# Kernel optimization log

Measured on AMD Instinct MI355X. Metric: run time of the kernel, lower is better.

The kernel has to match this reference:

```python
import jax, jax.numpy as jnp
import numpy as np

S, B, N, H = 64, 32, 325, 64

def setup_inputs() -> dict:
    key = jax.random.key(0)
    k1, k2, k3, k4 = jax.random.split(key, 4)
    return {
        "encoder_outputs": jax.random.normal(k1, (S, B, N, H), dtype=jnp.float32),
        "decoder_hidden": jax.random.normal(k2, (B, N, H), dtype=jnp.float32),
        "W": jax.random.normal(k3, (H, H), dtype=jnp.float32) * (1.0 / np.sqrt(H)),
        "b": jax.random.normal(k4, (H,), dtype=jnp.float32) * 0.01,
    }

def reference(encoder_outputs, decoder_hidden, W, b):
    # energy: (S,B,N,H) -- Linear + tanh
    energy = jnp.tanh(jnp.einsum('sbnh,kh->sbnk', encoder_outputs, W) + b)
    # broadcast multiply by decoder_hidden (B,N,H) and reduce over hidden dim -> (S,B,N)
    e = jnp.einsum('sbnh,bnh->sbn', energy, decoder_hidden)
    # softmax over seq_len, output (B,N,S)
    return jax.nn.softmax(jnp.transpose(e, (1, 2, 0)), axis=-1)
```

## Files before the change

### kernel.cpp

```cpp
#include <hip/hip_runtime.h>


constexpr int S = 64, B = 32, N = 325, H = 64;
constexpr int BN = B * N;

typedef __attribute__((ext_vector_type(8))) short short8;
typedef __attribute__((ext_vector_type(4))) float f32x4;

union FragU { unsigned u[4]; short8 s8; };

__device__ inline unsigned pack_hi(float x0, float x1, float& r0, float& r1) {
    unsigned u0 = __builtin_bit_cast(unsigned, x0);
    unsigned u1 = __builtin_bit_cast(unsigned, x1);
    r0 = x0 - __builtin_bit_cast(float, u0 & 0xffff0000u);
    r1 = x1 - __builtin_bit_cast(float, u1 & 0xffff0000u);
    return (u0 >> 16) | (u1 & 0xffff0000u);
}
__device__ inline unsigned pack_bf(float x0, float x1) {
    return (__builtin_bit_cast(unsigned, x0) >> 16) |
           (__builtin_bit_cast(unsigned, x1) & 0xffff0000u);
}

__global__ __launch_bounds__(256) void attn_mfma(
    const float* __restrict__ enc,
    const float* __restrict__ dec,
    const float* __restrict__ W,
    const float* __restrict__ bias,
    float* __restrict__ out)
{
    const int lane = threadIdx.x & 63;
    const int wv   = threadIdx.x >> 6;
    const int bn   = blockIdx.x * 4 + wv;
    const int col  = lane & 15;
    const int grp  = lane >> 4;

    __shared__ float P[4][16 * 65];
    float* Pw = P[wv];

    float bias_v[4], dec_v[4];
#pragma unroll
    for (int q = 0; q < 4; ++q) {
        bias_v[q] = bias[q * 16 + col];
        dec_v[q]  = dec[bn * H + q * 16 + col];
    }

    FragU a_hi[4][2], a_lo[4][2];
#pragma unroll
    for (int mt = 0; mt < 4; ++mt) {
        const float* er = enc + ((mt * 16 + col) * BN + bn) * H;
#pragma unroll
        for (int kc = 0; kc < 2; ++kc) {
            const float4* p4 = (const float4*)(er + kc * 32 + grp * 8);
            float4 x0 = p4[0], x1 = p4[1];
            float r0, r1, r2, r3, r4, r5, r6, r7;
            a_hi[mt][kc].u[0] = pack_hi(x0.x, x0.y, r0, r1);
            a_hi[mt][kc].u[1] = pack_hi(x0.z, x0.w, r2, r3);
            a_hi[mt][kc].u[2] = pack_hi(x1.x, x1.y, r4, r5);
            a_hi[mt][kc].u[3] = pack_hi(x1.z, x1.w, r6, r7);
            a_lo[mt][kc].u[0] = pack_bf(r0, r1);
            a_lo[mt][kc].u[1] = pack_bf(r2, r3);
            a_lo[mt][kc].u[2] = pack_bf(r4, r5);
            a_lo[mt][kc].u[3] = pack_bf(r6, r7);
        }
    }

    float e_s = 0.0f;

    for (int q = 0; q < 4; ++q) {
        f32x4 acc[4];
#pragma unroll
        for (int mt = 0; mt < 4; ++mt) acc[mt] = (f32x4){0.f, 0.f, 0.f, 0.f};

#pragma unroll
        for (int kc = 0; kc < 2; ++kc) {
            const float4* wp = (const float4*)(W + (q * 16 + col) * H + kc * 32 + grp * 8);
            float4 w0 = wp[0], w1 = wp[1];
            float r0, r1, r2, r3, r4, r5, r6, r7;
            FragU b_hi, b_lo;
            b_hi.u[0] = pack_hi(w0.x, w0.y, r0, r1);
            b_hi.u[1] = pack_hi(w0.z, w0.w, r2, r3);
            b_hi.u[2] = pack_hi(w1.x, w1.y, r4, r5);
            b_hi.u[3] = pack_hi(w1.z, w1.w, r6, r7);
            b_lo.u[0] = pack_bf(r0, r1);
            b_lo.u[1] = pack_bf(r2, r3);
            b_lo.u[2] = pack_bf(r4, r5);
            b_lo.u[3] = pack_bf(r6, r7);
#pragma unroll
            for (int mt = 0; mt < 4; ++mt) {
                acc[mt] = __builtin_amdgcn_mfma_f32_16x16x32_bf16(a_hi[mt][kc].s8, b_hi.s8, acc[mt], 0, 0, 0);
                acc[mt] = __builtin_amdgcn_mfma_f32_16x16x32_bf16(a_lo[mt][kc].s8, b_hi.s8, acc[mt], 0, 0, 0);
                acc[mt] = __builtin_amdgcn_mfma_f32_16x16x32_bf16(a_hi[mt][kc].s8, b_lo.s8, acc[mt], 0, 0, 0);
            }
        }

#pragma unroll
        for (int mt = 0; mt < 4; ++mt) {
#pragma unroll
            for (int r = 0; r < 4; ++r) {
                int s   = mt * 16 + grp * 4 + r;
                float a = acc[mt][r] + bias_v[q];
                float t = 1.0f - 2.0f * __builtin_amdgcn_rcpf(__expf(2.0f * a) + 1.0f);
                Pw[col * 65 + s] = t * dec_v[q];
            }
        }
#pragma unroll
        for (int k = 0; k < 16; ++k)
            e_s += Pw[k * 65 + lane];
    }

    float m = e_s;
#pragma unroll
    for (int off = 32; off > 0; off >>= 1)
        m = fmaxf(m, __shfl_xor(m, off, 64));
    float p = __expf(e_s - m);
    float sum = p;
#pragma unroll
    for (int off = 32; off > 0; off >>= 1)
        sum += __shfl_xor(sum, off, 64);

    out[bn * S + lane] = p * __builtin_amdgcn_rcpf(sum);
}

extern "C" void kernel_launch(void* const* d_in, const int* in_sizes, int n_in,
                              void* d_out, int out_size, void* d_ws, size_t ws_size,
                              hipStream_t stream) {
    const float* enc  = (const float*)d_in[0];
    const float* dec  = (const float*)d_in[1];
    const float* W    = (const float*)d_in[2];
    const float* bias = (const float*)d_in[3];
    float* out        = (float*)d_out;

    dim3 grid(BN / 4);
    attn_mfma<<<grid, 256, 0, stream>>>(enc, dec, W, bias, out);
}
```

Before: 263.8 us.

## Split sequence across wave pairs and prepack W fragments in a separate kernel

Each (b,n) row is now handled by two waves, each covering half of the sequence positions, so there are twice as many waves and fewer A-fragment registers per wave. The partial scores are combined through shared memory before the softmax. W is split into hi/lo bf16 fragments once by a small pre-kernel into workspace, which removes the per-block repacking. The cost is an extra kernel launch, a block-wide sync, and redundant softmax work on the second wave.

```diff
diff --git a/kernel.cpp b/kernel.cpp
--- a/kernel.cpp
+++ b/kernel.cpp
@@ -7,7 +7,7 @@
 typedef __attribute__((ext_vector_type(8))) short short8;
 typedef __attribute__((ext_vector_type(4))) float f32x4;
 
-union FragU { unsigned u[4]; short8 s8; };
+union FragU { unsigned u[4]; short8 s8; uint4 v4; };
 
 __device__ inline unsigned pack_hi(float x0, float x1, float& r0, float& r1) {
     unsigned u0 = __builtin_bit_cast(unsigned, x0);
@@ -21,20 +21,46 @@
            (__builtin_bit_cast(unsigned, x1) & 0xffff0000u);
 }
 
-__global__ __launch_bounds__(256) void attn_mfma(
+__global__ void pack_w(const float* __restrict__ W, uint4* __restrict__ wp) {
+    int idx  = blockIdx.x * blockDim.x + threadIdx.x;
+    if (idx >= 512) return;
+    int q    = idx >> 7;
+    int kc   = (idx >> 6) & 1;
+    int lane = idx & 63;
+    int col  = lane & 15, grp = lane >> 4;
+    const float4* wpt = (const float4*)(W + (q * 16 + col) * H + kc * 32 + grp * 8);
+    float4 w0 = wpt[0], w1 = wpt[1];
+    float r0, r1, r2, r3, r4, r5, r6, r7;
+    FragU hi, lo;
+    hi.u[0] = pack_hi(w0.x, w0.y, r0, r1);
+    hi.u[1] = pack_hi(w0.z, w0.w, r2, r3);
+    hi.u[2] = pack_hi(w1.x, w1.y, r4, r5);
+    hi.u[3] = pack_hi(w1.z, w1.w, r6, r7);
+    lo.u[0] = pack_bf(r0, r1);
+    lo.u[1] = pack_bf(r2, r3);
+    lo.u[2] = pack_bf(r4, r5);
+    lo.u[3] = pack_bf(r6, r7);
+    wp[((q * 2 + kc) * 2 + 0) * 64 + lane] = hi.v4;
+    wp[((q * 2 + kc) * 2 + 1) * 64 + lane] = lo.v4;
+}
+
+__global__ __launch_bounds__(256) void attn_mfma2(
     const float* __restrict__ enc,
     const float* __restrict__ dec,
-    const float* __restrict__ W,
     const float* __restrict__ bias,
+    const uint4* __restrict__ wp,
     float* __restrict__ out)
 {
-    const int lane = threadIdx.x & 63;
-    const int wv   = threadIdx.x >> 6;
-    const int bn   = blockIdx.x * 4 + wv;
-    const int col  = lane & 15;
-    const int grp  = lane >> 4;
+    const int lane  = threadIdx.x & 63;
+    const int wv    = threadIdx.x >> 6;
+    const int bnl   = wv >> 1;
+    const int shalf = wv & 1;
+    const int bn    = blockIdx.x * 2 + bnl;
+    const int col   = lane & 15;
+    const int grp   = lane >> 4;
 
-    __shared__ float P[4][16 * 65];
+    __shared__ float P[4][16 * 33];
+    __shared__ float eS[2][64];
     float* Pw = P[wv];
 
     float bias_v[4], dec_v[4];
@@ -44,10 +70,10 @@
         dec_v[q]  = dec[bn * H + q * 16 + col];
     }
 
-    FragU a_hi[4][2], a_lo[4][2];
+    FragU a_hi[2][2], a_lo[2][2];
 #pragma unroll
-    for (int mt = 0; mt < 4; ++mt) {
-        const float* er = enc + ((mt * 16 + col) * BN + bn) * H;
+    for (int mt = 0; mt < 2; ++mt) {
+        const float* er = enc + (((shalf * 2 + mt) * 16 + col) * BN + bn) * H;
 #pragma unroll
         for (int kc = 0; kc < 2; ++kc) {
             const float4* p4 = (const float4*)(er + kc * 32 + grp * 8);
@@ -65,60 +91,56 @@
     }
 
     float e_s = 0.0f;
-
+#pragma unroll
     for (int q = 0; q < 4; ++q) {
-        f32x4 acc[4];
+        f32x4 acc[2];
 #pragma unroll
-        for (int mt = 0; mt < 4; ++mt) acc[mt] = (f32x4){0.f, 0.f, 0.f, 0.f};
+        for (int mt = 0; mt < 2; ++mt) acc[mt] = (f32x4){0.f, 0.f, 0.f, 0.f};
 
 #pragma unroll
         for (int kc = 0; kc < 2; ++kc) {
-            const float4* wp = (const float4*)(W + (q * 16 + col) * H + kc * 32 + grp * 8);
-            float4 w0 = wp[0], w1 = wp[1];
-            float r0, r1, r2, r3, r4, r5, r6, r7;
-            FragU b_hi, b_lo;
-            b_hi.u[0] = pack_hi(w0.x, w0.y, r0, r1);
-            b_hi.u[1] = pack_hi(w0.z, w0.w, r2, r3);
-            b_hi.u[2] = pack_hi(w1.x, w1.y, r4, r5);
-            b_hi.u[3] = pack_hi(w1.z, w1.w, r6, r7);
-            b_lo.u[0] = pack_bf(r0, r1);
-            b_lo.u[1] = pack_bf(r2, r3);
-            b_lo.u[2] = pack_bf(r4, r5);
-            b_lo.u[3] = pack_bf(r6, r7);
+            FragU bh, bl;
+            bh.v4 = wp[((q * 2 + kc) * 2 + 0) * 64 + lane];
+            bl.v4 = wp[((q * 2 + kc) * 2 + 1) * 64 + lane];
 #pragma unroll
-            for (int mt = 0; mt < 4; ++mt) {
-                acc[mt] = __builtin_amdgcn_mfma_f32_16x16x32_bf16(a_hi[mt][kc].s8, b_hi.s8, acc[mt], 0, 0, 0);
-                acc[mt] = __builtin_amdgcn_mfma_f32_16x16x32_bf16(a_lo[mt][kc].s8, b_hi.s8, acc[mt], 0, 0, 0);
-                acc[mt] = __builtin_amdgcn_mfma_f32_16x16x32_bf16(a_hi[mt][kc].s8, b_lo.s8, acc[mt], 0, 0, 0);
+            for (int mt = 0; mt < 2; ++mt) {
+                acc[mt] = __builtin_amdgcn_mfma_f32_16x16x32_bf16(a_hi[mt][kc].s8, bh.s8, acc[mt], 0, 0, 0);
+                acc[mt] = __builtin_amdgcn_mfma_f32_16x16x32_bf16(a_lo[mt][kc].s8, bh.s8, acc[mt], 0, 0, 0);
+                acc[mt] = __builtin_amdgcn_mfma_f32_16x16x32_bf16(a_hi[mt][kc].s8, bl.s8, acc[mt], 0, 0, 0);
             }
         }
 
 #pragma unroll
-        for (int mt = 0; mt < 4; ++mt) {
+        for (int mt = 0; mt < 2; ++mt) {
 #pragma unroll
             for (int r = 0; r < 4; ++r) {
-                int s   = mt * 16 + grp * 4 + r;
+                int sl  = mt * 16 + grp * 4 + r;
                 float a = acc[mt][r] + bias_v[q];
                 float t = 1.0f - 2.0f * __builtin_amdgcn_rcpf(__expf(2.0f * a) + 1.0f);
-                Pw[col * 65 + s] = t * dec_v[q];
+                Pw[col * 33 + sl] = t * dec_v[q];
             }
         }
 #pragma unroll
         for (int k = 0; k < 16; ++k)
-            e_s += Pw[k * 65 + lane];
+            e_s += Pw[k * 33 + (lane & 31)];
     }
 
-    float m = e_s;
+    if (lane < 32) eS[bnl][shalf * 32 + lane] = e_s;
+    __syncthreads();
+    float ev = eS[bnl][lane];
+
+    float m = ev;
 #pragma unroll
     for (int off = 32; off > 0; off >>= 1)
         m = fmaxf(m, __shfl_xor(m, off, 64));
-    float p = __expf(e_s - m);
+    float p = __expf(ev - m);
     float sum = p;
 #pragma unroll
     for (int off = 32; off > 0; off >>= 1)
         sum += __shfl_xor(sum, off, 64);
 
-    out[bn * S + lane] = p * __builtin_amdgcn_rcpf(sum);
+    if (shalf == 0)
+        out[bn * S + lane] = p * __builtin_amdgcn_rcpf(sum);
 }
 
 extern "C" void kernel_launch(void* const* d_in, const int* in_sizes, int n_in,
@@ -130,6 +152,6 @@
     const float* bias = (const float*)d_in[3];
     float* out        = (float*)d_out;
 
-    dim3 grid(BN / 4);
-    attn_mfma<<<grid, 256, 0, stream>>>(enc, dec, W, bias, out);
+    pack_w<<<2, 256, 0, stream>>>(W, (uint4*)d_ws);
+    attn_mfma2<<<BN / 2, 256, 0, stream>>>(enc, dec, bias, (const uint4*)d_ws, out);
 }
```

Measured after the change: 257.9 us. -2.2%, faster.
